# Kernel tuning notes

Measured on AMD Instinct MI355X. Metric: run time of the kernel, lower is better.

The kernel has to match this reference:

```python
import jax, jax.numpy as jnp
import numpy as np

GROUPS = 32
K = 5          # up_kernel_size
UP = 2         # up_factor
EPS = 1e-5


def group_norm(x, w, b):
    B, C, H, W = x.shape
    xr = x.reshape(B, GROUPS, -1)
    mu = xr.mean(axis=2, keepdims=True)
    var = xr.var(axis=2, keepdims=True)
    xr = (xr - mu) * jax.lax.rsqrt(var + EPS)
    return xr.reshape(B, C, H, W) * w[None, :, None, None] + b[None, :, None, None]


def setup_inputs() -> dict:
    key = jax.random.key(0)
    ks = jax.random.split(key, 4)
    B, Cy, Cx, E, H, W = 4, 256, 256, 32, 64, 64
    return {
        "y": jax.random.normal(ks[0], (B, Cy, H * UP, W * UP), jnp.float32),
        "x": jax.random.normal(ks[1], (B, Cx, H, W), jnp.float32),
        "gn_y_w": jnp.ones((Cy,), jnp.float32),
        "gn_y_b": jnp.zeros((Cy,), jnp.float32),
        "gn_x_w": jnp.ones((Cx,), jnp.float32),
        "gn_x_b": jnp.zeros((Cx,), jnp.float32),
        "q_w": jax.random.normal(ks[2], (E, Cy), jnp.float32) * 0.02,
        "q_b": jnp.zeros((E,), jnp.float32),
        "k_w": jax.random.normal(ks[3], (E, Cx), jnp.float32) * 0.02,
        "k_b": jnp.zeros((E,), jnp.float32),
    }


def reference(y, x, gn_y_w, gn_y_b, gn_x_w, gn_x_b, q_w, q_b, k_w, k_b):
    pad = K // 2
    yn = group_norm(y, gn_y_w, gn_y_b)
    xn = group_norm(x, gn_x_w, gn_x_b)
    # 1x1 convs
    q = jnp.einsum('bchw,ec->behw', yn, q_w) + q_b[None, :, None, None]  # [B,E,Hu,Wu]
    k = jnp.einsum('bchw,ec->behw', xn, k_w) + k_b[None, :, None, None]  # [B,E,H,W]
    B, E, H, W = k.shape
    C = x.shape[1]
    # view q as per-low-res-cell blocks of UPxUP high-res queries
    q_r = q.reshape(B, E, H, UP, W, UP)
    k_pad = jnp.pad(k, ((0, 0), (0, 0), (pad, pad), (pad, pad)))  # zero pad (out-of-range -> 0 logit)
    v_pad = jnp.pad(x, ((0, 0), (0, 0), (pad, pad), (pad, pad)))
    # qk: logits over the KxK window (loop over 25 fixed offsets, vectorized inside)
    logits = []
    for dy in range(K):
        for dx in range(K):
            ks = k_pad[:, :, dy:dy + H, dx:dx + W]            # [B,E,H,W]
            logits.append(jnp.einsum('behuwv,behw->bhuwv', q_r, ks))
    logits = jnp.stack(logits, axis=1)                        # [B,KK,H,u,W,u]
    attn = jax.nn.softmax(logits, axis=1)
    # av: weighted aggregation of v over the same window
    out = jnp.zeros((B, C, H, UP, W, UP), x.dtype)
    idx = 0
    for dy in range(K):
        for dx in range(K):
            vs = v_pad[:, :, dy:dy + H, dx:dx + W]            # [B,C,H,W]
            out = out + attn[:, idx][:, None] * vs[:, :, :, None, :, None]
            idx += 1
    return out.reshape(B, C, H * UP, W * UP)
```

## Files before the change

kernel.cpp:

```cpp
#include <hip/hip_runtime.h>

#define EPSV 1e-5f

__global__ __launch_bounds__(256) void stats_kernel(const float* __restrict__ y,
                                                    const float* __restrict__ x,
                                                    float* __restrict__ part) {
    int bid = blockIdx.x;
    const float* src = (bid < 1024) ? (y + (size_t)bid * 16384)
                                    : (x + (size_t)(bid - 1024) * 16384);
    const float4* p = (const float4*)src;
    float s = 0.f, ss = 0.f;
    #pragma unroll 8
    for (int i = threadIdx.x; i < 4096; i += 256) {
        float4 v = p[i];
        s  += v.x + v.y + v.z + v.w;
        ss += v.x*v.x + v.y*v.y + v.z*v.z + v.w*v.w;
    }
    for (int off = 32; off > 0; off >>= 1) {
        s  += __shfl_down(s, off);
        ss += __shfl_down(ss, off);
    }
    __shared__ float red[8];
    int wid = threadIdx.x >> 6, lane = threadIdx.x & 63;
    if (lane == 0) { red[wid*2] = s; red[wid*2+1] = ss; }
    __syncthreads();
    if (threadIdx.x == 0) {
        part[bid*2+0] = red[0] + red[2] + red[4] + red[6];
        part[bid*2+1] = red[1] + red[3] + red[5] + red[7];
    }
}

__global__ __launch_bounds__(64) void make_eff_kernel(const float* __restrict__ qw, const float* __restrict__ qb,
                                                      const float* __restrict__ gyw, const float* __restrict__ gyb,
                                                      const float* __restrict__ kw, const float* __restrict__ kb,
                                                      const float* __restrict__ gxw, const float* __restrict__ gxb,
                                                      const float* __restrict__ part,
                                                      float* __restrict__ WeffQ, float* __restrict__ beffQ,
                                                      float* __restrict__ WeffK, float* __restrict__ beffK) {
    int id = blockIdx.x;
    int isK = id >> 7, b = (id >> 5) & 3, e = id & 31;
    const float* w     = isK ? kw  : qw;
    const float* bias  = isK ? kb  : qb;
    const float* gamma = isK ? gxw : gyw;
    const float* beta  = isK ? gxb : gyb;
    float inv_n = isK ? (1.f/32768.f) : (1.f/131072.f);
    float* W  = isK ? WeffK : WeffQ;
    float* be = isK ? beffK : beffQ;
    float partial = 0.f;
    for (int c = threadIdx.x; c < 256; c += 64) {
        int g = c >> 3, grp = b*32 + g;
        float s = 0.f, ss = 0.f;
        if (isK) {
            #pragma unroll
            for (int k2 = 0; k2 < 2; ++k2) {
                s  += part[(1024 + grp*2 + k2)*2 + 0];
                ss += part[(1024 + grp*2 + k2)*2 + 1];
            }
        } else {
            #pragma unroll
            for (int k2 = 0; k2 < 8; ++k2) {
                s  += part[(grp*8 + k2)*2 + 0];
                ss += part[(grp*8 + k2)*2 + 1];
            }
        }
        float mu = s * inv_n;
        float rs = rsqrtf(fmaf(-mu, mu, ss * inv_n) + EPSV);
        float wc = w[e*256 + c];
        float weff = wc * gamma[c] * rs;
        W[((size_t)b*256 + c)*32 + e] = weff;
        partial += wc * beta[c] - weff * mu;
    }
    for (int off = 32; off > 0; off >>= 1) partial += __shfl_down(partial, off);
    if (threadIdx.x == 0) be[b*32 + e] = partial + bias[e];
}

__global__ __launch_bounds__(256) void proj_kernel(const float* __restrict__ y, const float* __restrict__ x,
                                                   const float* __restrict__ WeffQ, const float* __restrict__ beffQ,
                                                   const float* __restrict__ WeffK, const float* __restrict__ beffK,
                                                   float* __restrict__ qbuf, float* __restrict__ kbuf) {
    int bid = blockIdx.x;
    int isX = bid >= 512;
    int lb = isX ? bid - 512 : bid;
    int b    = isX ? (lb >> 5) : (lb >> 7);
    int pxb  = isX ? (lb & 31) : (lb & 127);
    int npix = isX ? 4096 : 16384;
    const float* src   = isX ? x : y;
    const float* WeffT = isX ? WeffK : WeffQ;
    const float* beff  = isX ? beffK : beffQ;
    float* dst = isX ? kbuf : qbuf;

    int pix0 = pxb * 128 + (threadIdx.x & 63) * 2;
    int eg = __builtin_amdgcn_readfirstlane(threadIdx.x >> 6);
    const float* wp = WeffT + (size_t)b*256*32 + eg*8;
    float acc[2][8];
    #pragma unroll
    for (int j = 0; j < 8; ++j) {
        float bv = beff[b*32 + eg*8 + j];
        acc[0][j] = bv; acc[1][j] = bv;
    }
    const float* ysrc = src + (size_t)b*256*npix + pix0;
    #pragma unroll 8
    for (int c = 0; c < 256; ++c) {
        float2 t = *(const float2*)(ysrc + (size_t)c*npix);
        #pragma unroll
        for (int j = 0; j < 8; ++j) {
            float wj = wp[c*32 + j];
            acc[0][j] = fmaf(t.x, wj, acc[0][j]);
            acc[1][j] = fmaf(t.y, wj, acc[1][j]);
        }
    }
    float* dbase = dst + ((size_t)b*npix + pix0)*32 + eg*8;
    #pragma unroll
    for (int px = 0; px < 2; ++px) {
        float4 o0 = {acc[px][0], acc[px][1], acc[px][2], acc[px][3]};
        float4 o1 = {acc[px][4], acc[px][5], acc[px][6], acc[px][7]};
        *(float4*)(dbase + px*32 + 0) = o0;
        *(float4*)(dbase + px*32 + 4) = o1;
    }
}

__global__ __launch_bounds__(256) void attn_weights_kernel(const float* __restrict__ q,
                                                           const float* __restrict__ kk,
                                                           float* __restrict__ g_attn)
{
    __shared__ __align__(16) float sK[5184];
    __shared__ __align__(16) float sA[6400];
    int h0 = blockIdx.y * 8, w0 = blockIdx.x * 8;
    int b = blockIdx.z;
    int tid = threadIdx.x;

    for (int i = tid; i < 1152; i += 256) {
        int pos = i >> 3, e4 = i & 7;
        int r = pos / 12, c = pos - 12*r;
        int gh = h0 + r - 2, gw = w0 + c - 2;
        float4 v = make_float4(0.f, 0.f, 0.f, 0.f);
        if (gh >= 0 && gh < 64 && gw >= 0 && gw < 64)
            v = *(const float4*)(kk + (((size_t)b*4096 + gh*64 + gw)*32 + e4*4));
        *(float4*)&sK[pos*36 + e4*4] = v;
    }

    int h = tid >> 5, u = (tid >> 4) & 1, w = (tid >> 1) & 7, v = tid & 1;

    float qv[32];
    {
        int hh = 2*(h0 + h) + u, ww = 2*(w0 + w) + v;
        const float4* qp = (const float4*)(q + (((size_t)b*16384 + hh*128 + ww)*32));
        #pragma unroll
        for (int i4 = 0; i4 < 8; ++i4) {
            float4 t = qp[i4];
            qv[i4*4+0]=t.x; qv[i4*4+1]=t.y; qv[i4*4+2]=t.z; qv[i4*4+3]=t.w;
        }
    }
    __syncthreads();

    float a[25];
    const float* kbase = &sK[(h*12 + w)*36];
    #pragma unroll
    for (int j = 0; j < 25; ++j) {
        int dy = j / 5, dx = j - 5*dy;
        const float4* kp = (const float4*)(kbase + (dy*12 + dx)*36);
        float acc = 0.f;
        #pragma unroll
        for (int e4 = 0; e4 < 8; ++e4) {
            float4 kv = kp[e4];
            acc = fmaf(qv[e4*4+0], kv.x, acc);
            acc = fmaf(qv[e4*4+1], kv.y, acc);
            acc = fmaf(qv[e4*4+2], kv.z, acc);
            acc = fmaf(qv[e4*4+3], kv.w, acc);
        }
        a[j] = acc;
    }
    {
        float m = -1e30f;
        #pragma unroll
        for (int j = 0; j < 25; ++j) m = fmaxf(m, a[j]);
        float s = 0.f;
        #pragma unroll
        for (int j = 0; j < 25; ++j) { a[j] = __expf(a[j] - m); s += a[j]; }
        float inv = 1.f / s;
        #pragma unroll
        for (int j = 0; j < 25; ++j) sA[tid*25 + j] = a[j] * inv;
    }
    __syncthreads();

    float4* gdst = (float4*)(g_attn + ((size_t)b*64 + blockIdx.y*8 + blockIdx.x)*6400);
    const float4* ssrc = (const float4*)sA;
    for (int i = tid; i < 1600; i += 256) gdst[i] = ssrc[i];
}

__global__ __launch_bounds__(256) void gather_kernel(const float* __restrict__ g_attn,
                                                     const float* __restrict__ x,
                                                     float* __restrict__ out)
{
    __shared__ __align__(16) float sAttn[6400];
    __shared__ __align__(16) float sX[2880];
    int h0 = blockIdx.y * 8, w0 = blockIdx.x * 8;
    int b = blockIdx.z >> 2, slab = blockIdx.z & 3;
    int tid = threadIdx.x;

    {
        const float4* gsrc = (const float4*)(g_attn + ((size_t)b*64 + blockIdx.y*8 + blockIdx.x)*6400);
        float4* sdst = (float4*)sAttn;
        for (int i = tid; i < 1600; i += 256) sdst[i] = gsrc[i];
    }
    __syncthreads();

    float a[25];
    #pragma unroll
    for (int j = 0; j < 25; ++j) a[j] = sAttn[tid*25 + j];

    int h = tid >> 5, u = (tid >> 4) & 1, w = (tid >> 1) & 7, v = tid & 1;
    int hh = 2*(h0 + h) + u, ww = 2*(w0 + w) + v;
    int vbase = (h*12 + w)*20;

    for (int c0 = 0; c0 < 64; c0 += 16) {
        if (c0) __syncthreads();
        for (int i = 0; i < 9; ++i) {
            int t = i*256 + tid;
            int cc = t / 144, pos = t - 144*cc;
            int r = pos / 12, cl = pos - 12*r;
            int gh = h0 + r - 2, gw = w0 + cl - 2;
            float val = 0.f;
            if (gh >= 0 && gh < 64 && gw >= 0 && gw < 64)
                val = x[(((size_t)b*256 + slab*64 + c0 + cc)*64 + gh)*64 + gw];
            sX[pos*20 + cc] = val;
        }
        __syncthreads();

        #pragma unroll
        for (int g = 0; g < 4; ++g) {
            float o0 = 0.f, o1 = 0.f, o2 = 0.f, o3 = 0.f;
            const float* xb = &sX[vbase + g*4];
            #pragma unroll
            for (int j = 0; j < 25; ++j) {
                int dy = j / 5, dx = j - 5*dy;
                float4 xv = *(const float4*)(xb + (dy*12 + dx)*20);
                float aw = a[j];
                o0 = fmaf(aw, xv.x, o0);
                o1 = fmaf(aw, xv.y, o1);
                o2 = fmaf(aw, xv.z, o2);
                o3 = fmaf(aw, xv.w, o3);
            }
            size_t ob = (((size_t)b*256 + slab*64 + c0 + g*4)*128 + hh)*128 + ww;
            out[ob]           = o0;
            out[ob + 16384]   = o1;
            out[ob + 32768]   = o2;
            out[ob + 49152]   = o3;
        }
    }
}

extern "C" void kernel_launch(void* const* d_in, const int* in_sizes, int n_in,
                              void* d_out, int out_size, void* d_ws, size_t ws_size,
                              hipStream_t stream) {
    const float* y   = (const float*)d_in[0];
    const float* x   = (const float*)d_in[1];
    const float* gyw = (const float*)d_in[2];
    const float* gyb = (const float*)d_in[3];
    const float* gxw = (const float*)d_in[4];
    const float* gxb = (const float*)d_in[5];
    const float* qw  = (const float*)d_in[6];
    const float* qb  = (const float*)d_in[7];
    const float* kw  = (const float*)d_in[8];
    const float* kb  = (const float*)d_in[9];
    float* out = (float*)d_out;
    float* ws  = (float*)d_ws;

    float* part   = ws;
    float* WeffQ  = ws + 2560;
    float* beffQ  = ws + 35328;
    float* WeffK  = ws + 35456;
    float* beffK  = ws + 68224;
    float* qbuf   = ws + 68352;
    float* kbuf   = ws + 2165504;
    float* attnbf = ws + 2689792;

    stats_kernel<<<1280, 256, 0, stream>>>(y, x, part);
    make_eff_kernel<<<256, 64, 0, stream>>>(qw, qb, gyw, gyb, kw, kb, gxw, gxb,
                                            part, WeffQ, beffQ, WeffK, beffK);
    proj_kernel<<<640, 256, 0, stream>>>(y, x, WeffQ, beffQ, WeffK, beffK, qbuf, kbuf);
    attn_weights_kernel<<<dim3(8, 8, 4), 256, 0, stream>>>(qbuf, kbuf, attnbf);
    gather_kernel<<<dim3(8, 8, 16), 256, 0, stream>>>(attnbf, x, out);
}
```

Measured before the change: 213.1 us.

## Pack FMAs, split attention logits over 512 threads, restructure gather for vector stores

The projection kernel now uses two-wide float vectors so the compiler can emit packed FMAs. The attention-weights kernel runs 512 threads, each computing half of the 25 logits into padded shared memory, then 256 threads do the softmax. The gather kernel loads all 64 channels of its x halo once instead of in four chunks. It reads attention weights straight from global memory, and each thread handles two horizontal sub-pixels so stores become float2. The larger shared tile lowers occupancy, and the padded attention buffer adds some extra traffic.

```diff
diff --git a/kernel.cpp b/kernel.cpp
--- a/kernel.cpp
+++ b/kernel.cpp
@@ -1,6 +1,8 @@
 #include <hip/hip_runtime.h>
 
 #define EPSV 1e-5f
+
+typedef float f32x2 __attribute__((ext_vector_type(2)));
 
 __global__ __launch_bounds__(256) void stats_kernel(const float* __restrict__ y,
                                                     const float* __restrict__ x,
@@ -92,44 +94,41 @@
     int pix0 = pxb * 128 + (threadIdx.x & 63) * 2;
     int eg = __builtin_amdgcn_readfirstlane(threadIdx.x >> 6);
     const float* wp = WeffT + (size_t)b*256*32 + eg*8;
-    float acc[2][8];
+    f32x2 acc[8];
     #pragma unroll
     for (int j = 0; j < 8; ++j) {
         float bv = beff[b*32 + eg*8 + j];
-        acc[0][j] = bv; acc[1][j] = bv;
+        acc[j] = (f32x2){bv, bv};
     }
     const float* ysrc = src + (size_t)b*256*npix + pix0;
     #pragma unroll 8
     for (int c = 0; c < 256; ++c) {
-        float2 t = *(const float2*)(ysrc + (size_t)c*npix);
-        #pragma unroll
-        for (int j = 0; j < 8; ++j) {
-            float wj = wp[c*32 + j];
-            acc[0][j] = fmaf(t.x, wj, acc[0][j]);
-            acc[1][j] = fmaf(t.y, wj, acc[1][j]);
-        }
+        f32x2 t = *(const f32x2*)(ysrc + (size_t)c*npix);
+        #pragma unroll
+        for (int j = 0; j < 8; ++j)
+            acc[j] += t * wp[c*32 + j];
     }
     float* dbase = dst + ((size_t)b*npix + pix0)*32 + eg*8;
     #pragma unroll
     for (int px = 0; px < 2; ++px) {
-        float4 o0 = {acc[px][0], acc[px][1], acc[px][2], acc[px][3]};
-        float4 o1 = {acc[px][4], acc[px][5], acc[px][6], acc[px][7]};
+        float4 o0 = {acc[0][px], acc[1][px], acc[2][px], acc[3][px]};
+        float4 o1 = {acc[4][px], acc[5][px], acc[6][px], acc[7][px]};
         *(float4*)(dbase + px*32 + 0) = o0;
         *(float4*)(dbase + px*32 + 4) = o1;
     }
 }
 
-__global__ __launch_bounds__(256) void attn_weights_kernel(const float* __restrict__ q,
+__global__ __launch_bounds__(512) void attn_weights_kernel(const float* __restrict__ q,
                                                            const float* __restrict__ kk,
                                                            float* __restrict__ g_attn)
 {
     __shared__ __align__(16) float sK[5184];
-    __shared__ __align__(16) float sA[6400];
+    __shared__ __align__(16) float sA[7168];
     int h0 = blockIdx.y * 8, w0 = blockIdx.x * 8;
     int b = blockIdx.z;
     int tid = threadIdx.x;
 
-    for (int i = tid; i < 1152; i += 256) {
+    for (int i = tid; i < 1152; i += 512) {
         int pos = i >> 3, e4 = i & 7;
         int r = pos / 12, c = pos - 12*r;
         int gh = h0 + r - 2, gw = w0 + c - 2;
@@ -139,7 +138,8 @@
         *(float4*)&sK[pos*36 + e4*4] = v;
     }
 
-    int h = tid >> 5, u = (tid >> 4) & 1, w = (tid >> 1) & 7, v = tid & 1;
+    int cid = tid & 255, half = tid >> 8;
+    int h = cid >> 5, u = (cid >> 4) & 1, w = (cid >> 1) & 7, v = cid & 1;
 
     float qv[32];
     {
@@ -153,10 +153,10 @@
     }
     __syncthreads();
 
-    float a[25];
+    int jlo = half ? 13 : 0;
+    int jhi = half ? 25 : 13;
     const float* kbase = &sK[(h*12 + w)*36];
-    #pragma unroll
-    for (int j = 0; j < 25; ++j) {
+    for (int j = jlo; j < jhi; ++j) {
         int dy = j / 5, dx = j - 5*dy;
         const float4* kp = (const float4*)(kbase + (dy*12 + dx)*36);
         float acc = 0.f;
@@ -168,84 +168,93 @@
             acc = fmaf(qv[e4*4+2], kv.z, acc);
             acc = fmaf(qv[e4*4+3], kv.w, acc);
         }
-        a[j] = acc;
-    }
-    {
-        float m = -1e30f;
-        #pragma unroll
-        for (int j = 0; j < 25; ++j) m = fmaxf(m, a[j]);
+        sA[cid*28 + j] = acc;
+    }
+    __syncthreads();
+
+    if (tid < 256) {
+        float a[25], m = -1e30f;
+        #pragma unroll
+        for (int j = 0; j < 25; ++j) { a[j] = sA[tid*28 + j]; m = fmaxf(m, a[j]); }
         float s = 0.f;
         #pragma unroll
         for (int j = 0; j < 25; ++j) { a[j] = __expf(a[j] - m); s += a[j]; }
         float inv = 1.f / s;
         #pragma unroll
-        for (int j = 0; j < 25; ++j) sA[tid*25 + j] = a[j] * inv;
-    }
-    __syncthreads();
-
-    float4* gdst = (float4*)(g_attn + ((size_t)b*64 + blockIdx.y*8 + blockIdx.x)*6400);
+        for (int j = 0; j < 25; ++j) sA[tid*28 + j] = a[j] * inv;
+        sA[tid*28 + 25] = 0.f; sA[tid*28 + 26] = 0.f; sA[tid*28 + 27] = 0.f;
+    }
+    __syncthreads();
+
+    float4* gdst = (float4*)(g_attn + ((size_t)b*64 + blockIdx.y*8 + blockIdx.x)*7168);
     const float4* ssrc = (const float4*)sA;
-    for (int i = tid; i < 1600; i += 256) gdst[i] = ssrc[i];
+    for (int i = tid; i < 1792; i += 512) gdst[i] = ssrc[i];
 }
 
 __global__ __launch_bounds__(256) void gather_kernel(const float* __restrict__ g_attn,
                                                      const float* __restrict__ x,
                                                      float* __restrict__ out)
 {
-    __shared__ __align__(16) float sAttn[6400];
-    __shared__ __align__(16) float sX[2880];
+    __shared__ __align__(16) float sX[9792];
     int h0 = blockIdx.y * 8, w0 = blockIdx.x * 8;
     int b = blockIdx.z >> 2, slab = blockIdx.z & 3;
     int tid = threadIdx.x;
 
-    {
-        const float4* gsrc = (const float4*)(g_attn + ((size_t)b*64 + blockIdx.y*8 + blockIdx.x)*6400);
-        float4* sdst = (float4*)sAttn;
-        for (int i = tid; i < 1600; i += 256) sdst[i] = gsrc[i];
-    }
-    __syncthreads();
-
-    float a[25];
+    #pragma unroll 4
+    for (int i = 0; i < 36; ++i) {
+        int t = i*256 + tid;
+        int cc = t / 144, pos = t - 144*cc;
+        int r = pos / 12, cl = pos - 12*r;
+        int gh = h0 + r - 2, gw = w0 + cl - 2;
+        float val = 0.f;
+        if (gh >= 0 && gh < 64 && gw >= 0 && gw < 64)
+            val = x[(((size_t)b*256 + slab*64 + cc)*64 + gh)*64 + gw];
+        sX[pos*68 + cc] = val;
+    }
+    __syncthreads();
+
+    int p = tid & 63, ci = tid >> 6;
+    int pw = p & 7, ph = p >> 3;
+    const float* tbase = g_attn + ((size_t)b*64 + blockIdx.y*8 + blockIdx.x)*7168;
+    const float* xb0 = &sX[(ph*12 + pw)*68];
+    int ww = 2*(w0 + pw);
+
     #pragma unroll
-    for (int j = 0; j < 25; ++j) a[j] = sAttn[tid*25 + j];
-
-    int h = tid >> 5, u = (tid >> 4) & 1, w = (tid >> 1) & 7, v = tid & 1;
-    int hh = 2*(h0 + h) + u, ww = 2*(w0 + w) + v;
-    int vbase = (h*12 + w)*20;
-
-    for (int c0 = 0; c0 < 64; c0 += 16) {
-        if (c0) __syncthreads();
-        for (int i = 0; i < 9; ++i) {
-            int t = i*256 + tid;
-            int cc = t / 144, pos = t - 144*cc;
-            int r = pos / 12, cl = pos - 12*r;
-            int gh = h0 + r - 2, gw = w0 + cl - 2;
-            float val = 0.f;
-            if (gh >= 0 && gh < 64 && gw >= 0 && gw < 64)
-                val = x[(((size_t)b*256 + slab*64 + c0 + cc)*64 + gh)*64 + gw];
-            sX[pos*20 + cc] = val;
-        }
-        __syncthreads();
-
-        #pragma unroll
-        for (int g = 0; g < 4; ++g) {
-            float o0 = 0.f, o1 = 0.f, o2 = 0.f, o3 = 0.f;
-            const float* xb = &sX[vbase + g*4];
+    for (int u = 0; u < 2; ++u) {
+        float a2[2][25];
+        #pragma unroll
+        for (int v = 0; v < 2; ++v) {
+            const float4* ap = (const float4*)(tbase + (32*ph + 16*u + 2*pw + v)*28);
+            float tmp[28];
+            #pragma unroll
+            for (int q4 = 0; q4 < 7; ++q4) *(float4*)&tmp[q4*4] = ap[q4];
+            #pragma unroll
+            for (int j = 0; j < 25; ++j) a2[v][j] = tmp[j];
+        }
+        int hh = 2*(h0 + ph) + u;
+
+        #pragma unroll
+        for (int c0i = 0; c0i < 4; ++c0i) {
+            int cc = c0i*16 + ci*4;
+            const float* xb = xb0 + cc;
+            f32x2 acc00 = {0.f,0.f}, acc01 = {0.f,0.f};
+            f32x2 acc10 = {0.f,0.f}, acc11 = {0.f,0.f};
             #pragma unroll
             for (int j = 0; j < 25; ++j) {
                 int dy = j / 5, dx = j - 5*dy;
-                float4 xv = *(const float4*)(xb + (dy*12 + dx)*20);
-                float aw = a[j];
-                o0 = fmaf(aw, xv.x, o0);
-                o1 = fmaf(aw, xv.y, o1);
-                o2 = fmaf(aw, xv.z, o2);
-                o3 = fmaf(aw, xv.w, o3);
+                float4 xv = *(const float4*)(xb + (dy*12 + dx)*68);
+                f32x2 x01 = {xv.x, xv.y}, x23 = {xv.z, xv.w};
+                acc00 += x01 * a2[0][j];
+                acc01 += x23 * a2[0][j];
+                acc10 += x01 * a2[1][j];
+                acc11 += x23 * a2[1][j];
             }
-            size_t ob = (((size_t)b*256 + slab*64 + c0 + g*4)*128 + hh)*128 + ww;
-            out[ob]           = o0;
-            out[ob + 16384]   = o1;
-            out[ob + 32768]   = o2;
-            out[ob + 49152]   = o3;
+            int c = slab*64 + cc;
+            size_t ob = (((size_t)b*256 + c)*128 + hh)*128 + ww;
+            *(float2*)(out + ob)           = make_float2(acc00.x, acc10.x);
+            *(float2*)(out + ob + 16384)   = make_float2(acc00.y, acc10.y);
+            *(float2*)(out + ob + 32768)   = make_float2(acc01.x, acc11.x);
+            *(float2*)(out + ob + 49152)   = make_float2(acc01.y, acc11.y);
         }
     }
 }
@@ -279,6 +288,6 @@
     make_eff_kernel<<<256, 64, 0, stream>>>(qw, qb, gyw, gyb, kw, kb, gxw, gxb,
                                             part, WeffQ, beffQ, WeffK, beffK);
     proj_kernel<<<640, 256, 0, stream>>>(y, x, WeffQ, beffQ, WeffK, beffK, qbuf, kbuf);
-    attn_weights_kernel<<<dim3(8, 8, 4), 256, 0, stream>>>(qbuf, kbuf, attnbf);
+    attn_weights_kernel<<<dim3(8, 8, 4), 512, 0, stream>>>(qbuf, kbuf, attnbf);
     gather_kernel<<<dim3(8, 8, 16), 256, 0, stream>>>(attnbf, x, out);
 }
```

Result: slower. 260.0 us (+22.0%).
